# Kernel optimization log

Measured on AMD Instinct MI355X. Metric: run time of the kernel, lower is better.

The kernel has to match this reference:

```python
import jax, jax.numpy as jnp
import numpy as np

B, L, LQ = 64, 4096, 128
D = 32        # input_dim (value channels)
ET = 128      # embed_time
NH = 1        # num_heads
H = 128       # nhidden
NC = 6        # n_classes


def _time_emb(tt, lin_w, lin_b, per_w, per_b):
    # tt [..., T] -> [..., T, ET]; cat(Linear(1,1)(t), sin(Linear(1,ET-1)(t)))
    tt = tt[..., None]
    out1 = tt * lin_w[0, 0] + lin_b
    out2 = jnp.sin(tt @ per_w + per_b)
    return jnp.concatenate([out1, out2], axis=-1)


def _gru_dir(xs, wih, whh, bih, bhh, reverse):
    # xs [B, T, I] -> [B, T, H]; torch GRU gate math
    xs_t = jnp.swapaxes(xs, 0, 1)              # [T, B, I]
    if reverse:
        xs_t = xs_t[::-1]
    gi_all = xs_t @ wih.T + bih                # [T, B, 3H] precomputed input gates
    h0 = jnp.zeros((xs.shape[0], H), xs.dtype)

    def step(h, gi):
        gh = h @ whh.T + bhh
        ir, iz, inn = jnp.split(gi, 3, axis=-1)
        hr, hz, hn = jnp.split(gh, 3, axis=-1)
        r = jax.nn.sigmoid(ir + hr)
        z = jax.nn.sigmoid(iz + hz)
        n = jnp.tanh(inn + r * hn)
        h_new = (1.0 - z) * n + z * h
        return h_new, h_new

    _, ys = jax.lax.scan(step, h0, gi_all)     # [T, B, H]
    if reverse:
        ys = ys[::-1]
    return jnp.swapaxes(ys, 0, 1)


def _bigru(xs, wih, whh, bih, bhh):
    fwd = _gru_dir(xs, wih[0], whh[0], bih[0], bhh[0], False)
    bwd = _gru_dir(xs, wih[1], whh[1], bih[1], bhh[1], True)
    return jnp.concatenate([fwd, bwd], axis=-1)


def setup_inputs() -> dict:
    ks = jax.random.split(jax.random.key(0), 32)
    w = lambda i, s: jax.random.normal(ks[i], s, jnp.float32) * 0.05
    G3 = 3 * H
    return {
        "x": jax.random.normal(ks[0], (B, L, D), jnp.float32),
        "time_steps": jax.random.uniform(ks[1], (B, L), dtype=jnp.float32),
        "query_times": jnp.linspace(0.0, 1.0, LQ, dtype=jnp.float32),
        "lin_w": w(2, (1, 1)), "lin_b": w(3, (1,)),
        "per_w": w(4, (1, ET - 1)), "per_b": w(5, (ET - 1,)),
        "wq": w(6, (ET, ET)), "bq": w(7, (ET,)),
        "wk": w(8, (ET, ET)), "bk": w(9, (ET,)),
        "wo": w(10, (NH * D, H)), "bo": w(11, (H,)),
        "gru0_wih": w(12, (2, G3, H)), "gru0_whh": w(13, (2, G3, H)),
        "gru0_bih": w(14, (2, G3)), "gru0_bhh": w(15, (2, G3)),
        "gru1_wih": w(16, (2, G3, 2 * H)), "gru1_whh": w(17, (2, G3, H)),
        "gru1_bih": w(18, (2, G3)), "gru1_bhh": w(19, (2, G3)),
        "c1_w": w(20, (2 * H, 128)), "c1_b": w(21, (128,)),
        "c2_w": w(22, (128, 64)), "c2_b": w(23, (64,)),
        "c3_w": w(24, (64, NC)), "c3_b": w(25, (NC,)),
    }


def reference(x, time_steps, query_times, lin_w, lin_b, per_w, per_b,
              wq, bq, wk, bk, wo, bo,
              gru0_wih, gru0_whh, gru0_bih, gru0_bhh,
              gru1_wih, gru1_whh, gru1_bih, gru1_bhh,
              c1_w, c1_b, c2_w, c2_b, c3_w, c3_b):
    ek = ET // NH
    # learned time embeddings
    q = _time_emb(query_times[None, :], lin_w, lin_b, per_w, per_b)  # [1, LQ, ET]
    k = _time_emb(time_steps, lin_w, lin_b, per_w, per_b)            # [B, L, ET]
    # per-head projections
    qp = (q @ wq + bq).reshape(1, LQ, NH, ek).transpose(0, 2, 1, 3)[0]  # [NH, LQ, ek]
    kp = (k @ wk + bk).reshape(B, L, NH, ek).transpose(0, 2, 1, 3)      # [B, NH, L, ek]
    # mTAN attention: scores are channel-independent (mask=None), so the
    # per-channel repeat+softmax reduces to a single softmax over keys.
    scores = jnp.einsum('hqe,bhke->bhqk', qp, kp) / jnp.sqrt(jnp.float32(ek))
    p = jax.nn.softmax(scores, axis=-1)                                 # [B, NH, LQ, L]
    att = jnp.einsum('bhqk,bkd->bqhd', p, x).reshape(B, LQ, NH * D)
    att_out = att @ wo + bo                                             # [B, LQ, H]
    # 2-layer bidirectional GRU
    g0 = _bigru(att_out, gru0_wih, gru0_whh, gru0_bih, gru0_bhh)        # [B, LQ, 2H]
    g1 = _bigru(g0, gru1_wih, gru1_whh, gru1_bih, gru1_bhh)             # [B, LQ, 2H]
    class_in = jnp.concatenate([g1[:, -1, :H], g1[:, 0, H:]], axis=1)   # [B, 2H]
    out = ((class_in @ c1_w + c1_b) @ c2_w + c2_b) @ c3_w + c3_b        # [B, NC]
    return out
```

## Files before the change

kernel.cpp:

```cpp
#include <hip/hip_runtime.h>
#include <math.h>

#define Bn   64
#define Ln   4096
#define LQn  128
#define Dn   32
#define ETn  128
#define Hn   128
#define G3n  384
#define NDEG 12

typedef __attribute__((ext_vector_type(2))) float f32x2;
typedef __attribute__((ext_vector_type(2))) _Float16 f16x2;

#define DPPF(x, ctrl) __int_as_float(__builtin_amdgcn_update_dpp(0, __float_as_int(x), (ctrl), 0xF, 0xF, true))
#define QP_XOR1 0xB1
#define QP_XOR2 0x4E
#define QP_B0   0x00
#define QP_B1   0x55
#define QP_B2   0xAA
#define QP_B3   0xFF

__device__ __forceinline__ float sin_poly(float x) {
    const float x2 = x * x;
    float r = -1.9841270114e-04f;
    r = fmaf(r, x2,  8.3333337680e-03f);
    r = fmaf(r, x2, -1.6666667163e-01f);
    return fmaf(r * x2, x, x);
}
__device__ __forceinline__ float cos_poly(float x) {
    const float x2 = x * x;
    float r =  2.4801587642e-05f;
    r = fmaf(r, x2, -1.3888888899e-03f);
    r = fmaf(r, x2,  4.1666667908e-02f);
    r = fmaf(r, x2, -5.0000000000e-01f);
    return fmaf(r, x2, 1.0f);
}

#define WS_C    0
#define WS_WT   4096
#define WS_B2   (WS_WT + 768*32)
#define WS_CLS  (WS_B2 + 1024)
#define WS_G0   (WS_CLS + Bn*2*Hn)
#define WS_GI   (WS_G0 + Bn*LQn*2*Hn)
#define WS_ACCP WS_G0
#define WS_SP   (WS_G0 + 1048576)

__global__ __launch_bounds__(128) void k_coef(
    const float* __restrict__ qtimes, const float* __restrict__ lin_w,
    const float* __restrict__ lin_b, const float* __restrict__ per_w,
    const float* __restrict__ per_b, const float* __restrict__ wq,
    const float* __restrict__ bq, const float* __restrict__ wk,
    const float* __restrict__ bk, float* __restrict__ C)
{
    __shared__ float qe[ETn], qp_l[ETn], qt_l[ETn], bas[NDEG * 128], red[96], qbk_red[32];
    const int q = blockIdx.x, tid = threadIdx.x;
    if (tid < ETn - 1) {
        const float w = per_w[tid], bb = per_b[tid];
        const float sb = sin_poly(bb), cb = cos_poly(bb);
        float wp = 1.f;
#pragma unroll
        for (int d = 0; d < NDEG; ++d) {
            const float sd = ((d & 3) == 0) ? sb : ((d & 3) == 1) ? cb : ((d & 3) == 2) ? -sb : -cb;
            bas[d * 128 + tid] = wp * sd;
            wp *= w / (float)(d + 1);
        }
    }
    const float t = qtimes[q];
    qe[tid] = (tid == 0) ? fmaf(t, lin_w[0], lin_b[0])
                         : sin_poly(fmaf(t, per_w[tid - 1], per_b[tid - 1]));
    __syncthreads();
    {
        float a = bq[tid];
#pragma unroll 16
        for (int i = 0; i < ETn; ++i) a = fmaf(qe[i], wq[i * ETn + tid], a);
        qp_l[tid] = a;
    }
    __syncthreads();
    {
        const float4* wk4 = (const float4*)(wk + (size_t)tid * ETn);
        const float4* qp4 = (const float4*)qp_l;
        float a = 0.f;
#pragma unroll
        for (int k = 0; k < 32; ++k) {
            const float4 w4 = wk4[k], p4 = qp4[k];
            a += w4.x * p4.x + w4.y * p4.y + w4.z * p4.z + w4.w * p4.w;
        }
        qt_l[tid] = a;
    }
    __syncthreads();
    if (tid < 96) {
        const int d = tid >> 3, g = tid & 7;
        float p = 0.f;
        for (int j = g; j < ETn - 1; j += 8) p = fmaf(qt_l[j + 1], bas[d * 128 + j], p);
        red[tid] = p;
    } else {
        const int g2 = tid - 96;
        float p = 0.f;
#pragma unroll
        for (int k = 0; k < 4; ++k) p = fmaf(qp_l[g2 + 32 * k], bk[g2 + 32 * k], p);
        qbk_red[g2] = p;
    }
    __syncthreads();
    if (tid < NDEG) {
        const int d = tid;
        float s = red[d * 8 + 0] + red[d * 8 + 1] + red[d * 8 + 2] + red[d * 8 + 3]
                + red[d * 8 + 4] + red[d * 8 + 5] + red[d * 8 + 6] + red[d * 8 + 7];
        if (d == 0) {
            float qbk = 0.f;
#pragma unroll
            for (int k = 0; k < 32; ++k) qbk += qbk_red[k];
            s += qt_l[0] * lin_b[0] + qbk;
        }
        if (d == 1) s += qt_l[0] * lin_w[0];
        C[q * NDEG + d] = s * 0.08838834764831845f;
    }
}

__global__ __launch_bounds__(256) void k_fuse(
    const float* __restrict__ wih, const float* __restrict__ wo,
    const float* __restrict__ bo, const float* __restrict__ bih,
    float* __restrict__ Wt, float* __restrict__ bias2)
{
    const int t = blockIdx.x * 256 + threadIdx.x;
    if (t < 768 * 32) {
        const int o = t >> 5, d = t & 31;
        const float4* wr4 = (const float4*)(wih + (size_t)o * 128);
        const float4* wc4 = (const float4*)(wo + (size_t)d * 128);
        float a = 0.f;
#pragma unroll
        for (int k = 0; k < 32; ++k) {
            const float4 r4 = wr4[k], c4 = wc4[k];
            a += r4.x * c4.x + r4.y * c4.y + r4.z * c4.z + r4.w * c4.w;
        }
        Wt[t] = a;
    } else if (t < 768 * 33) {
        const int o = t - 768 * 32;
        const float4* wr4 = (const float4*)(wih + (size_t)o * 128);
        const float4* bo4 = (const float4*)bo;
        float a = bih[o];
#pragma unroll
        for (int k = 0; k < 32; ++k) {
            const float4 r4 = wr4[k], b4 = bo4[k];
            a += r4.x * b4.x + r4.y * b4.y + r4.z * b4.z + r4.w * b4.w;
        }
        bias2[o] = a;
    }
}

__global__ __launch_bounds__(512, 1) void k_attn(
    const float* __restrict__ x, const float* __restrict__ tsteps,
    const float* __restrict__ Cc, float* __restrict__ accP, float* __restrict__ sP)
{
    __shared__ float4 xls[4 * 64 * 8];
    __shared__ float  slab[4][128][36];
    const int tid = threadIdx.x;
    const int b = blockIdx.x >> 2, lsplit = blockIdx.x & 3;
    const int i = tid & 3, qt = (tid >> 2) & 31, ls2 = tid >> 7;
    const int qown = 4 * qt + i;
    const int u = tid & 127;

    float c[NDEG];
#pragma unroll
    for (int d = 0; d < NDEG; ++d) c[d] = Cc[qown * NDEG + d];

    const int l0 = lsplit * 1024 + ls2 * 256;
    const float4* tg4 = (const float4*)(tsteps + (size_t)b * Ln + l0);
    const float4* xg  = (const float4*)(x + ((size_t)b * Ln + l0) * Dn);

    f32x2 acc2[4][4];
#pragma unroll
    for (int m = 0; m < 4; ++m)
#pragma unroll
        for (int e = 0; e < 4; ++e) { acc2[m][e].x = 0.f; acc2[m][e].y = 0.f; }
    float s_own = 0.f;

    float4 xr[4];
#pragma unroll
    for (int w = 0; w < 4; ++w) xr[w] = xg[u + 128 * w];

    for (int ch = 0; ch < 4; ++ch) {
        __syncthreads();
#pragma unroll
        for (int w = 0; w < 4; ++w) xls[ls2 * 512 + u + 128 * w] = xr[w];
        __syncthreads();
        if (ch < 3) {
            const int off = (ch + 1) * 512;
#pragma unroll
            for (int w = 0; w < 4; ++w) xr[w] = xg[off + u + 128 * w];
        }
        const float4* xrow = &xls[ls2 * 512];
        for (int k = 0; k < 16; ++k) {
            const float4 t4 = tg4[ch * 16 + k];
#pragma unroll
            for (int jj = 0; jj < 4; ++jj) {
                const float t = (jj == 0) ? t4.x : (jj == 1) ? t4.y : (jj == 2) ? t4.z : t4.w;
                float sc = c[NDEG - 1];
#pragma unroll
                for (int d = NDEG - 2; d >= 0; --d) sc = fmaf(sc, t, c[d]);
                const float pe = __expf(sc);
                s_own += pe;
                const float p0 = DPPF(pe, QP_B0);
                const float p1 = DPPF(pe, QP_B1);
                const float p2 = DPPF(pe, QP_B2);
                const float p3 = DPPF(pe, QP_B3);
                const int lrow = (k * 4 + jj) * 8;
                const float4 xa = xrow[lrow + 2 * i];
                const float4 xb = xrow[lrow + 2 * i + 1];
                f32x2 xa0; xa0.x = xa.x; xa0.y = xa.y;
                f32x2 xa1; xa1.x = xa.z; xa1.y = xa.w;
                f32x2 xb0; xb0.x = xb.x; xb0.y = xb.y;
                f32x2 xb1; xb1.x = xb.z; xb1.y = xb.w;
#define PKA(m, pv) { f32x2 pp; pp.x = (pv); pp.y = (pv); \
    acc2[m][0] = __builtin_elementwise_fma(pp, xa0, acc2[m][0]); \
    acc2[m][1] = __builtin_elementwise_fma(pp, xa1, acc2[m][1]); \
    acc2[m][2] = __builtin_elementwise_fma(pp, xb0, acc2[m][2]); \
    acc2[m][3] = __builtin_elementwise_fma(pp, xb1, acc2[m][3]); }
                PKA(0, p0) PKA(1, p1) PKA(2, p2) PKA(3, p3)
#undef PKA
            }
        }
    }
    __syncthreads();
#pragma unroll
    for (int m = 0; m < 4; ++m) {
        float4 f4a, f4b;
        f4a.x = acc2[m][0].x; f4a.y = acc2[m][0].y; f4a.z = acc2[m][1].x; f4a.w = acc2[m][1].y;
        f4b.x = acc2[m][2].x; f4b.y = acc2[m][2].y; f4b.z = acc2[m][3].x; f4b.w = acc2[m][3].y;
        *(float4*)&slab[ls2][4 * qt + m][8 * i]     = f4a;
        *(float4*)&slab[ls2][4 * qt + m][8 * i + 4] = f4b;
    }
    slab[ls2][qown][32] = s_own;
    __syncthreads();
    const int q = tid & 127, part = tid >> 7;
#pragma unroll
    for (int j = 0; j < 2; ++j) {
        const int off = (part * 2 + j) * 4;
        float4 r  = *(float4*)&slab[0][q][off];
        float4 r1 = *(float4*)&slab[1][q][off];
        float4 r2 = *(float4*)&slab[2][q][off];
        float4 r3 = *(float4*)&slab[3][q][off];
        r.x += r1.x + r2.x + r3.x; r.y += r1.y + r2.y + r3.y;
        r.z += r1.z + r2.z + r3.z; r.w += r1.w + r2.w + r3.w;
        *(float4*)&accP[((((size_t)lsplit * Bn + b) * LQn + q) * 32) + off] = r;
    }
    if (part == 0) {
        sP[((size_t)lsplit * Bn + b) * LQn + q] =
            slab[0][q][32] + slab[1][q][32] + slab[2][q][32] + slab[3][q][32];
    }
}

__global__ __launch_bounds__(256) void k_gemm_att(
    const float* __restrict__ accP, const float* __restrict__ sP,
    const float* __restrict__ Bm, const float* __restrict__ bias,
    float* __restrict__ Cm)
{
    __shared__ float4 A_l[64 * 8];
    __shared__ float4 B_l[64 * 8];
    const int tid = threadIdx.x;
    const int m0 = blockIdx.x * 64, n0 = blockIdx.y * 64;
    const int r0 = (tid >> 4) << 2, c0 = (tid & 15) << 2;
    f32x2 acc2[4][4];
#pragma unroll
    for (int a = 0; a < 4; ++a)
#pragma unroll
        for (int bb = 0; bb < 4; ++bb) { acc2[a][bb].x = 0.f; acc2[a][bb].y = 0.f; }
    const float4* Ag = (const float4*)accP;
    const float4* Bg = (const float4*)Bm;

#pragma unroll
    for (int w = 0; w < 2; ++w) {
        const int idx = tid + w * 256;
        const int row = idx >> 3, c4 = idx & 7;
        const int sc = (c4 + row + (row >> 2)) & 7;
        const int m = m0 + row;
        float4 a0 = Ag[(size_t)m * 8 + c4];
        float4 a1 = Ag[((size_t)8192  + m) * 8 + c4];
        float4 a2 = Ag[((size_t)16384 + m) * 8 + c4];
        float4 a3 = Ag[((size_t)24576 + m) * 8 + c4];
        const float inv = 1.f / (sP[m] + sP[8192 + m] + sP[16384 + m] + sP[24576 + m]);
        float4 av;
        av.x = (a0.x + a1.x + a2.x + a3.x) * inv;
        av.y = (a0.y + a1.y + a2.y + a3.y) * inv;
        av.z = (a0.z + a1.z + a2.z + a3.z) * inv;
        av.w = (a0.w + a1.w + a2.w + a3.w) * inv;
        A_l[row * 8 + sc] = av;
        B_l[row * 8 + sc] = Bg[(size_t)(n0 + row) * 8 + c4];
    }
    __syncthreads();
#pragma unroll
    for (int k4 = 0; k4 < 8; ++k4) {
        float4 av[4], bv[4];
#pragma unroll
        for (int j = 0; j < 4; ++j) {
            const int ra = r0 + j;
            av[j] = A_l[ra * 8 + ((k4 + ra + (ra >> 2)) & 7)];
        }
#pragma unroll
        for (int j = 0; j < 4; ++j) {
            const int rb = c0 + j;
            bv[j] = B_l[rb * 8 + ((k4 + rb + (rb >> 2)) & 7)];
        }
#pragma unroll
        for (int ri = 0; ri < 4; ++ri) {
            f32x2 alo; alo.x = av[ri].x; alo.y = av[ri].y;
            f32x2 ahi; ahi.x = av[ri].z; ahi.y = av[ri].w;
#pragma unroll
            for (int ci = 0; ci < 4; ++ci) {
                f32x2 blo; blo.x = bv[ci].x; blo.y = bv[ci].y;
                f32x2 bhi; bhi.x = bv[ci].z; bhi.y = bv[ci].w;
                acc2[ri][ci] = __builtin_elementwise_fma(alo, blo, acc2[ri][ci]);
                acc2[ri][ci] = __builtin_elementwise_fma(ahi, bhi, acc2[ri][ci]);
            }
        }
    }
#pragma unroll
    for (int ri = 0; ri < 4; ++ri) {
        float4 o4;
        o4.x = acc2[ri][0].x + acc2[ri][0].y + bias[n0 + c0 + 0];
        o4.y = acc2[ri][1].x + acc2[ri][1].y + bias[n0 + c0 + 1];
        o4.z = acc2[ri][2].x + acc2[ri][2].y + bias[n0 + c0 + 2];
        o4.w = acc2[ri][3].x + acc2[ri][3].y + bias[n0 + c0 + 3];
        *(float4*)&Cm[(size_t)(m0 + r0 + ri) * 768 + n0 + c0] = o4;
    }
}

__global__ __launch_bounds__(256) void k_gemm_nt(
    const float* __restrict__ A, const float* __restrict__ Bm,
    const float* __restrict__ bias, float* __restrict__ Cm,
    int N, int K)
{
    __shared__ float4 A_l[64 * 8];
    __shared__ float4 B_l[64 * 8];
    const int tid = threadIdx.x;
    const int m0 = blockIdx.x * 64, n0 = blockIdx.y * 64;
    const int r0 = (tid >> 4) << 2, c0 = (tid & 15) << 2;
    const int K4 = K >> 2;
    f32x2 acc2[4][4];
#pragma unroll
    for (int a = 0; a < 4; ++a)
#pragma unroll
        for (int bb = 0; bb < 4; ++bb) { acc2[a][bb].x = 0.f; acc2[a][bb].y = 0.f; }
    const float4* Ag = (const float4*)A;
    const float4* Bg = (const float4*)Bm;

    for (int k0 = 0; k0 < K4; k0 += 8) {
        __syncthreads();
#pragma unroll
        for (int w = 0; w < 2; ++w) {
            const int idx = tid + w * 256;
            const int row = idx >> 3, c4 = idx & 7;
            const int sc = (c4 + row + (row >> 2)) & 7;
            A_l[row * 8 + sc] = Ag[(size_t)(m0 + row) * K4 + k0 + c4];
            B_l[row * 8 + sc] = Bg[(size_t)(n0 + row) * K4 + k0 + c4];
        }
        __syncthreads();
#pragma unroll
        for (int k4 = 0; k4 < 8; ++k4) {
            float4 av[4], bv[4];
#pragma unroll
            for (int j = 0; j < 4; ++j) {
                const int ra = r0 + j;
                av[j] = A_l[ra * 8 + ((k4 + ra + (ra >> 2)) & 7)];
            }
#pragma unroll
            for (int j = 0; j < 4; ++j) {
                const int rb = c0 + j;
                bv[j] = B_l[rb * 8 + ((k4 + rb + (rb >> 2)) & 7)];
            }
#pragma unroll
            for (int ri = 0; ri < 4; ++ri) {
                f32x2 alo; alo.x = av[ri].x; alo.y = av[ri].y;
                f32x2 ahi; ahi.x = av[ri].z; ahi.y = av[ri].w;
#pragma unroll
                for (int ci = 0; ci < 4; ++ci) {
                    f32x2 blo; blo.x = bv[ci].x; blo.y = bv[ci].y;
                    f32x2 bhi; bhi.x = bv[ci].z; bhi.y = bv[ci].w;
                    acc2[ri][ci] = __builtin_elementwise_fma(alo, blo, acc2[ri][ci]);
                    acc2[ri][ci] = __builtin_elementwise_fma(ahi, bhi, acc2[ri][ci]);
                }
            }
        }
    }
#pragma unroll
    for (int ri = 0; ri < 4; ++ri) {
        float4 o4;
        o4.x = acc2[ri][0].x + acc2[ri][0].y + bias[n0 + c0 + 0];
        o4.y = acc2[ri][1].x + acc2[ri][1].y + bias[n0 + c0 + 1];
        o4.z = acc2[ri][2].x + acc2[ri][2].y + bias[n0 + c0 + 2];
        o4.w = acc2[ri][3].x + acc2[ri][3].y + bias[n0 + c0 + 3];
        *(float4*)&Cm[(size_t)(m0 + r0 + ri) * N + n0 + c0] = o4;
    }
}

__global__ __launch_bounds__(256, 1) void k_gru(
    const float* __restrict__ gi, const float* __restrict__ whh,
    const float* __restrict__ bhh, float* __restrict__ seq_out,
    float* __restrict__ final_out)
{
    __shared__ _Float16 h16[2][Hn];
    __shared__ float    h32[2][Hn];
    const int tid = threadIdx.x;
    const int b = blockIdx.x >> 1, dir = blockIdx.x & 1;
    const int j = tid >> 1, q = tid & 1;

    f16x2 wr[32], wz[32], wn[32];
    {
        const float* wb = whh + ((size_t)dir * G3n + j) * Hn + 64 * q;
        const f32x2* p0 = (const f32x2*)(wb);
        const f32x2* p1 = (const f32x2*)(wb + (size_t)128 * Hn);
        const f32x2* p2 = (const f32x2*)(wb + (size_t)256 * Hn);
#pragma unroll
        for (int k = 0; k < 32; ++k) {
            f32x2 a = p0[k], z2 = p1[k], c2 = p2[k];
            wr[k].x = (_Float16)a.x;  wr[k].y = (_Float16)a.y;
            wz[k].x = (_Float16)z2.x; wz[k].y = (_Float16)z2.y;
            wn[k].x = (_Float16)c2.x; wn[k].y = (_Float16)c2.y;
        }
    }
#pragma unroll
    for (int k = 0; k < 32; ++k) {
        asm volatile("" : "+v"(wr[k]));
        asm volatile("" : "+v"(wz[k]));
        asm volatile("" : "+v"(wn[k]));
    }
    const float bhr = bhh[dir * G3n + j];
    const float bhz = bhh[dir * G3n + 128 + j];
    const float bhn = bhh[dir * G3n + 256 + j];

    if (tid < Hn) {
        h32[0][tid] = 0.f; h32[1][tid] = 0.f;
        h16[0][tid] = (_Float16)0.f; h16[1][tid] = (_Float16)0.f;
    }
    __syncthreads();

    const long sstride = dir ? -768 : 768;
    const float* gptr = gi + (size_t)b * LQn * 768 + dir * G3n + j
                        + (size_t)(dir ? LQn - 1 : 0) * 768;

    int cur = 0;
    float hlast = 0.f;

    auto gstep = [&](const float gir, const float giz, const float gin, const int step) {
        const float hold = h32[cur][j];
        const float4* hb4 = (const float4*)(&h16[cur][64 * q]);
        float sr = 0.f, sz = 0.f, sn = 0.f;
#pragma unroll
        for (int k2 = 0; k2 < 8; ++k2) {
            float4 hv = hb4[k2];
            f16x2 h0 = *(f16x2*)&hv.x;
            f16x2 h1 = *(f16x2*)&hv.y;
            f16x2 h2 = *(f16x2*)&hv.z;
            f16x2 h3 = *(f16x2*)&hv.w;
            asm("v_dot2_f32_f16 %0, %1, %2, %0" : "+v"(sr) : "v"(wr[4 * k2 + 0]), "v"(h0));
            asm("v_dot2_f32_f16 %0, %1, %2, %0" : "+v"(sz) : "v"(wz[4 * k2 + 0]), "v"(h0));
            asm("v_dot2_f32_f16 %0, %1, %2, %0" : "+v"(sn) : "v"(wn[4 * k2 + 0]), "v"(h0));
            asm("v_dot2_f32_f16 %0, %1, %2, %0" : "+v"(sr) : "v"(wr[4 * k2 + 1]), "v"(h1));
            asm("v_dot2_f32_f16 %0, %1, %2, %0" : "+v"(sz) : "v"(wz[4 * k2 + 1]), "v"(h1));
            asm("v_dot2_f32_f16 %0, %1, %2, %0" : "+v"(sn) : "v"(wn[4 * k2 + 1]), "v"(h1));
            asm("v_dot2_f32_f16 %0, %1, %2, %0" : "+v"(sr) : "v"(wr[4 * k2 + 2]), "v"(h2));
            asm("v_dot2_f32_f16 %0, %1, %2, %0" : "+v"(sz) : "v"(wz[4 * k2 + 2]), "v"(h2));
            asm("v_dot2_f32_f16 %0, %1, %2, %0" : "+v"(sn) : "v"(wn[4 * k2 + 2]), "v"(h2));
            asm("v_dot2_f32_f16 %0, %1, %2, %0" : "+v"(sr) : "v"(wr[4 * k2 + 3]), "v"(h3));
            asm("v_dot2_f32_f16 %0, %1, %2, %0" : "+v"(sz) : "v"(wz[4 * k2 + 3]), "v"(h3));
            asm("v_dot2_f32_f16 %0, %1, %2, %0" : "+v"(sn) : "v"(wn[4 * k2 + 3]), "v"(h3));
        }
        sr += DPPF(sr, QP_XOR1);
        sz += DPPF(sz, QP_XOR1);
        sn += DPPF(sn, QP_XOR1);
        const float r = 1.f / (1.f + __expf(-(gir + sr + bhr)));
        const float z = 1.f / (1.f + __expf(-(giz + sz + bhz)));
        const float nx = gin + r * (sn + bhn);
        const float n = 1.f - 2.f / (1.f + __expf(2.f * nx));
        const float hn = n + z * (hold - n);
        if (q == 0) {
            h32[cur ^ 1][j] = hn;
            h16[cur ^ 1][j] = (_Float16)hn;
            if (seq_out) {
                const int l = dir ? (LQn - 1 - step) : step;
                seq_out[((size_t)(b * LQn + l)) * (2 * Hn) + dir * Hn + j] = hn;
            }
        }
        hlast = hn;
        cur ^= 1;
        asm volatile("s_waitcnt lgkmcnt(0)\n\ts_barrier" ::: "memory");
    };

    float gA[3], gB[3];
#define GLD(dst, s) { const long o = (long)(s) * sstride; \
    dst[0] = gptr[o]; dst[1] = gptr[o + 128]; dst[2] = gptr[o + 256]; }
    GLD(gA, 0) GLD(gB, 1)
    for (int s0 = 0; s0 < LQn; s0 += 2) {
        gstep(gA[0], gA[1], gA[2], s0);
        { const int sn2 = (s0 + 2 < LQn) ? s0 + 2 : LQn - 1; GLD(gA, sn2) }
        gstep(gB[0], gB[1], gB[2], s0 + 1);
        { const int sn2 = (s0 + 3 < LQn) ? s0 + 3 : LQn - 1; GLD(gB, sn2) }
    }
#undef GLD
    if (final_out && q == 0) final_out[b * 2 * Hn + dir * Hn + j] = hlast;
}

__global__ __launch_bounds__(256) void k_cls(
    const float* __restrict__ cls_in,
    const float* __restrict__ c1w, const float* __restrict__ c1b,
    const float* __restrict__ c2w, const float* __restrict__ c2b,
    const float* __restrict__ c3w, const float* __restrict__ c3b,
    float* __restrict__ out)
{
    __shared__ float ci[256], y1[128], y2[64];
    const int b = blockIdx.x, tid = threadIdx.x;
    ci[tid] = cls_in[b * 256 + tid];
    __syncthreads();
    if (tid < 128) { float a = c1b[tid]; for (int i = 0; i < 256; ++i) a += ci[i] * c1w[i * 128 + tid]; y1[tid] = a; }
    __syncthreads();
    if (tid < 64)  { float a = c2b[tid]; for (int i = 0; i < 128; ++i) a += y1[i] * c2w[i * 64 + tid];  y2[tid] = a; }
    __syncthreads();
    if (tid < 6)   { float a = c3b[tid]; for (int i = 0; i < 64; ++i)  a += y2[i] * c3w[i * 6 + tid];   out[b * 6 + tid] = a; }
}

extern "C" void kernel_launch(void* const* d_in, const int* in_sizes, int n_in,
                              void* d_out, int out_size, void* d_ws, size_t ws_size,
                              hipStream_t stream)
{
    const float* x        = (const float*)d_in[0];
    const float* tsteps   = (const float*)d_in[1];
    const float* qtimes   = (const float*)d_in[2];
    const float* lin_w    = (const float*)d_in[3];
    const float* lin_b    = (const float*)d_in[4];
    const float* per_w    = (const float*)d_in[5];
    const float* per_b    = (const float*)d_in[6];
    const float* wq       = (const float*)d_in[7];
    const float* bq       = (const float*)d_in[8];
    const float* wk       = (const float*)d_in[9];
    const float* bk       = (const float*)d_in[10];
    const float* wo       = (const float*)d_in[11];
    const float* bo       = (const float*)d_in[12];
    const float* g0_wih   = (const float*)d_in[13];
    const float* g0_whh   = (const float*)d_in[14];
    const float* g0_bih   = (const float*)d_in[15];
    const float* g0_bhh   = (const float*)d_in[16];
    const float* g1_wih   = (const float*)d_in[17];
    const float* g1_whh   = (const float*)d_in[18];
    const float* g1_bih   = (const float*)d_in[19];
    const float* g1_bhh   = (const float*)d_in[20];
    const float* c1w      = (const float*)d_in[21];
    const float* c1b      = (const float*)d_in[22];
    const float* c2w      = (const float*)d_in[23];
    const float* c2b      = (const float*)d_in[24];
    const float* c3w      = (const float*)d_in[25];
    const float* c3b      = (const float*)d_in[26];
    float* out = (float*)d_out;
    float* ws  = (float*)d_ws;

    float* Cws   = ws + WS_C;
    float* Wt    = ws + WS_WT;
    float* bias2 = ws + WS_B2;
    float* clsin = ws + WS_CLS;
    float* g0buf = ws + WS_G0;
    float* accP  = ws + WS_ACCP;
    float* sPb   = ws + WS_SP;
    float* gibuf = ws + WS_GI;

    k_coef<<<128, 128, 0, stream>>>(qtimes, lin_w, lin_b, per_w, per_b, wq, bq, wk, bk, Cws);
    k_fuse<<<99, 256, 0, stream>>>(g0_wih, wo, bo, g0_bih, Wt, bias2);
    k_attn<<<256, 512, 0, stream>>>(x, tsteps, Cws, accP, sPb);

    k_gemm_att<<<dim3(128, 12), 256, 0, stream>>>(accP, sPb, Wt, bias2, gibuf);
    k_gru<<<128, 256, 0, stream>>>(gibuf, g0_whh, g0_bhh, g0buf, nullptr);

    k_gemm_nt<<<dim3(128, 12), 256, 0, stream>>>(g0buf, g1_wih, g1_bih, gibuf, 768, 256);
    k_gru<<<128, 256, 0, stream>>>(gibuf, g1_whh, g1_bhh, nullptr, clsin);

    k_cls<<<64, 256, 0, stream>>>(clsin, c1w, c1b, c2w, c2b, c3w, c3b, out);
}
```

Baseline: 302.3 us.

## Process two batch rows per GRU block and union attention shared memory

The GRU kernel now handles two batch elements per block. Each pair of lanes computes dot products for both batch rows against the same register-resident weights, and each lane then finalises the gates for its own row, so the grid halves from 128 to 64 blocks and the weight-load cost is shared. The attention kernel aliases its x staging buffer and its reduction slab into one shared-memory region and raises the launch-bounds occupancy hint to 4, lowering LDS use per block. The trade-off is twice the dot-product work per step in the latency-bound GRU recurrence, and the aliasing is correct only if the staging buffer is no longer read once the slab is written.

```diff
diff --git a/kernel.cpp b/kernel.cpp
--- a/kernel.cpp
+++ b/kernel.cpp
@@ -148,12 +148,14 @@
     }
 }
 
-__global__ __launch_bounds__(512, 1) void k_attn(
+__global__ __launch_bounds__(512, 4) void k_attn(
     const float* __restrict__ x, const float* __restrict__ tsteps,
     const float* __restrict__ Cc, float* __restrict__ accP, float* __restrict__ sP)
 {
-    __shared__ float4 xls[4 * 64 * 8];
-    __shared__ float  slab[4][128][36];
+    __shared__ __align__(16) char smem[4 * 128 * 36 * 4];
+    float4* xls  = (float4*)smem;
+    float*  slabf = (float*)smem;
+#define SLAB(s, qq, c) slabf[(((s) * 128) + (qq)) * 36 + (c)]
     const int tid = threadIdx.x;
     const int b = blockIdx.x >> 2, lsplit = blockIdx.x & 3;
     const int i = tid & 3, qt = (tid >> 2) & 31, ls2 = tid >> 7;
@@ -227,27 +229,28 @@
         float4 f4a, f4b;
         f4a.x = acc2[m][0].x; f4a.y = acc2[m][0].y; f4a.z = acc2[m][1].x; f4a.w = acc2[m][1].y;
         f4b.x = acc2[m][2].x; f4b.y = acc2[m][2].y; f4b.z = acc2[m][3].x; f4b.w = acc2[m][3].y;
-        *(float4*)&slab[ls2][4 * qt + m][8 * i]     = f4a;
-        *(float4*)&slab[ls2][4 * qt + m][8 * i + 4] = f4b;
-    }
-    slab[ls2][qown][32] = s_own;
+        *(float4*)&SLAB(ls2, 4 * qt + m, 8 * i)     = f4a;
+        *(float4*)&SLAB(ls2, 4 * qt + m, 8 * i + 4) = f4b;
+    }
+    SLAB(ls2, qown, 32) = s_own;
     __syncthreads();
     const int q = tid & 127, part = tid >> 7;
 #pragma unroll
     for (int j = 0; j < 2; ++j) {
         const int off = (part * 2 + j) * 4;
-        float4 r  = *(float4*)&slab[0][q][off];
-        float4 r1 = *(float4*)&slab[1][q][off];
-        float4 r2 = *(float4*)&slab[2][q][off];
-        float4 r3 = *(float4*)&slab[3][q][off];
+        float4 r  = *(float4*)&SLAB(0, q, off);
+        float4 r1 = *(float4*)&SLAB(1, q, off);
+        float4 r2 = *(float4*)&SLAB(2, q, off);
+        float4 r3 = *(float4*)&SLAB(3, q, off);
         r.x += r1.x + r2.x + r3.x; r.y += r1.y + r2.y + r3.y;
         r.z += r1.z + r2.z + r3.z; r.w += r1.w + r2.w + r3.w;
         *(float4*)&accP[((((size_t)lsplit * Bn + b) * LQn + q) * 32) + off] = r;
     }
     if (part == 0) {
         sP[((size_t)lsplit * Bn + b) * LQn + q] =
-            slab[0][q][32] + slab[1][q][32] + slab[2][q][32] + slab[3][q][32];
-    }
+            SLAB(0, q, 32) + SLAB(1, q, 32) + SLAB(2, q, 32) + SLAB(3, q, 32);
+    }
+#undef SLAB
 }
 
 __global__ __launch_bounds__(256) void k_gemm_att(
@@ -398,11 +401,12 @@
     const float* __restrict__ bhh, float* __restrict__ seq_out,
     float* __restrict__ final_out)
 {
-    __shared__ _Float16 h16[2][Hn];
-    __shared__ float    h32[2][Hn];
+    __shared__ _Float16 h16[2][2][Hn];
+    __shared__ float    h32[2][2][Hn];
     const int tid = threadIdx.x;
-    const int b = blockIdx.x >> 1, dir = blockIdx.x & 1;
+    const int bg = blockIdx.x >> 1, dir = blockIdx.x & 1;
     const int j = tid >> 1, q = tid & 1;
+    const int b = bg * 2 + q;
 
     f16x2 wr[32], wz[32], wn[32];
     {
@@ -428,58 +432,69 @@
     const float bhz = bhh[dir * G3n + 128 + j];
     const float bhn = bhh[dir * G3n + 256 + j];
 
-    if (tid < Hn) {
-        h32[0][tid] = 0.f; h32[1][tid] = 0.f;
-        h16[0][tid] = (_Float16)0.f; h16[1][tid] = (_Float16)0.f;
-    }
+    ((float*)h32)[tid] = 0.f;      ((float*)h32)[tid + 256] = 0.f;
+    ((_Float16*)h16)[tid] = (_Float16)0.f; ((_Float16*)h16)[tid + 256] = (_Float16)0.f;
     __syncthreads();
 
     const long sstride = dir ? -768 : 768;
-    const float* gptr = gi + (size_t)b * LQn * 768 + dir * G3n + j
-                        + (size_t)(dir ? LQn - 1 : 0) * 768;
+    const float* gptr = gi + ((size_t)b * LQn + (size_t)(dir ? LQn - 1 : 0)) * 768
+                        + dir * G3n + j;
 
     int cur = 0;
     float hlast = 0.f;
 
-    auto gstep = [&](const float gir, const float giz, const float gin, const int step) {
-        const float hold = h32[cur][j];
-        const float4* hb4 = (const float4*)(&h16[cur][64 * q]);
-        float sr = 0.f, sz = 0.f, sn = 0.f;
+    auto gstep = [&](const float g0, const float g1, const float g2, const int step) {
+        const float hold = h32[cur][q][j];
+        const float4* hb0 = (const float4*)(&h16[cur][0][64 * q]);
+        const float4* hb1 = (const float4*)(&h16[cur][1][64 * q]);
+        float sr0 = 0.f, sz0 = 0.f, sn0 = 0.f;
+        float sr1 = 0.f, sz1 = 0.f, sn1 = 0.f;
 #pragma unroll
         for (int k2 = 0; k2 < 8; ++k2) {
-            float4 hv = hb4[k2];
-            f16x2 h0 = *(f16x2*)&hv.x;
-            f16x2 h1 = *(f16x2*)&hv.y;
-            f16x2 h2 = *(f16x2*)&hv.z;
-            f16x2 h3 = *(f16x2*)&hv.w;
-            asm("v_dot2_f32_f16 %0, %1, %2, %0" : "+v"(sr) : "v"(wr[4 * k2 + 0]), "v"(h0));
-            asm("v_dot2_f32_f16 %0, %1, %2, %0" : "+v"(sz) : "v"(wz[4 * k2 + 0]), "v"(h0));
-            asm("v_dot2_f32_f16 %0, %1, %2, %0" : "+v"(sn) : "v"(wn[4 * k2 + 0]), "v"(h0));
-            asm("v_dot2_f32_f16 %0, %1, %2, %0" : "+v"(sr) : "v"(wr[4 * k2 + 1]), "v"(h1));
-            asm("v_dot2_f32_f16 %0, %1, %2, %0" : "+v"(sz) : "v"(wz[4 * k2 + 1]), "v"(h1));
-            asm("v_dot2_f32_f16 %0, %1, %2, %0" : "+v"(sn) : "v"(wn[4 * k2 + 1]), "v"(h1));
-            asm("v_dot2_f32_f16 %0, %1, %2, %0" : "+v"(sr) : "v"(wr[4 * k2 + 2]), "v"(h2));
-            asm("v_dot2_f32_f16 %0, %1, %2, %0" : "+v"(sz) : "v"(wz[4 * k2 + 2]), "v"(h2));
-            asm("v_dot2_f32_f16 %0, %1, %2, %0" : "+v"(sn) : "v"(wn[4 * k2 + 2]), "v"(h2));
-            asm("v_dot2_f32_f16 %0, %1, %2, %0" : "+v"(sr) : "v"(wr[4 * k2 + 3]), "v"(h3));
-            asm("v_dot2_f32_f16 %0, %1, %2, %0" : "+v"(sz) : "v"(wz[4 * k2 + 3]), "v"(h3));
-            asm("v_dot2_f32_f16 %0, %1, %2, %0" : "+v"(sn) : "v"(wn[4 * k2 + 3]), "v"(h3));
-        }
-        sr += DPPF(sr, QP_XOR1);
-        sz += DPPF(sz, QP_XOR1);
-        sn += DPPF(sn, QP_XOR1);
-        const float r = 1.f / (1.f + __expf(-(gir + sr + bhr)));
-        const float z = 1.f / (1.f + __expf(-(giz + sz + bhz)));
-        const float nx = gin + r * (sn + bhn);
+            const float4 v0 = hb0[k2];
+            const float4 v1 = hb1[k2];
+            f16x2 a0 = *(f16x2*)&v0.x, a1 = *(f16x2*)&v0.y, a2 = *(f16x2*)&v0.z, a3 = *(f16x2*)&v0.w;
+            f16x2 c0 = *(f16x2*)&v1.x, c1 = *(f16x2*)&v1.y, c2 = *(f16x2*)&v1.z, c3 = *(f16x2*)&v1.w;
+            asm("v_dot2_f32_f16 %0, %1, %2, %0" : "+v"(sr0) : "v"(wr[4 * k2 + 0]), "v"(a0));
+            asm("v_dot2_f32_f16 %0, %1, %2, %0" : "+v"(sz0) : "v"(wz[4 * k2 + 0]), "v"(a0));
+            asm("v_dot2_f32_f16 %0, %1, %2, %0" : "+v"(sn0) : "v"(wn[4 * k2 + 0]), "v"(a0));
+            asm("v_dot2_f32_f16 %0, %1, %2, %0" : "+v"(sr1) : "v"(wr[4 * k2 + 0]), "v"(c0));
+            asm("v_dot2_f32_f16 %0, %1, %2, %0" : "+v"(sz1) : "v"(wz[4 * k2 + 0]), "v"(c0));
+            asm("v_dot2_f32_f16 %0, %1, %2, %0" : "+v"(sn1) : "v"(wn[4 * k2 + 0]), "v"(c0));
+            asm("v_dot2_f32_f16 %0, %1, %2, %0" : "+v"(sr0) : "v"(wr[4 * k2 + 1]), "v"(a1));
+            asm("v_dot2_f32_f16 %0, %1, %2, %0" : "+v"(sz0) : "v"(wz[4 * k2 + 1]), "v"(a1));
+            asm("v_dot2_f32_f16 %0, %1, %2, %0" : "+v"(sn0) : "v"(wn[4 * k2 + 1]), "v"(a1));
+            asm("v_dot2_f32_f16 %0, %1, %2, %0" : "+v"(sr1) : "v"(wr[4 * k2 + 1]), "v"(c1));
+            asm("v_dot2_f32_f16 %0, %1, %2, %0" : "+v"(sz1) : "v"(wz[4 * k2 + 1]), "v"(c1));
+            asm("v_dot2_f32_f16 %0, %1, %2, %0" : "+v"(sn1) : "v"(wn[4 * k2 + 1]), "v"(c1));
+            asm("v_dot2_f32_f16 %0, %1, %2, %0" : "+v"(sr0) : "v"(wr[4 * k2 + 2]), "v"(a2));
+            asm("v_dot2_f32_f16 %0, %1, %2, %0" : "+v"(sz0) : "v"(wz[4 * k2 + 2]), "v"(a2));
+            asm("v_dot2_f32_f16 %0, %1, %2, %0" : "+v"(sn0) : "v"(wn[4 * k2 + 2]), "v"(a2));
+            asm("v_dot2_f32_f16 %0, %1, %2, %0" : "+v"(sr1) : "v"(wr[4 * k2 + 2]), "v"(c2));
+            asm("v_dot2_f32_f16 %0, %1, %2, %0" : "+v"(sz1) : "v"(wz[4 * k2 + 2]), "v"(c2));
+            asm("v_dot2_f32_f16 %0, %1, %2, %0" : "+v"(sn1) : "v"(wn[4 * k2 + 2]), "v"(c2));
+            asm("v_dot2_f32_f16 %0, %1, %2, %0" : "+v"(sr0) : "v"(wr[4 * k2 + 3]), "v"(a3));
+            asm("v_dot2_f32_f16 %0, %1, %2, %0" : "+v"(sz0) : "v"(wz[4 * k2 + 3]), "v"(a3));
+            asm("v_dot2_f32_f16 %0, %1, %2, %0" : "+v"(sn0) : "v"(wn[4 * k2 + 3]), "v"(a3));
+            asm("v_dot2_f32_f16 %0, %1, %2, %0" : "+v"(sr1) : "v"(wr[4 * k2 + 3]), "v"(c3));
+            asm("v_dot2_f32_f16 %0, %1, %2, %0" : "+v"(sz1) : "v"(wz[4 * k2 + 3]), "v"(c3));
+            asm("v_dot2_f32_f16 %0, %1, %2, %0" : "+v"(sn1) : "v"(wn[4 * k2 + 3]), "v"(c3));
+        }
+        sr0 += DPPF(sr0, QP_XOR1); sz0 += DPPF(sz0, QP_XOR1); sn0 += DPPF(sn0, QP_XOR1);
+        sr1 += DPPF(sr1, QP_XOR1); sz1 += DPPF(sz1, QP_XOR1); sn1 += DPPF(sn1, QP_XOR1);
+        const float sr = q ? sr1 : sr0;
+        const float sz = q ? sz1 : sz0;
+        const float sn = q ? sn1 : sn0;
+        const float r = 1.f / (1.f + __expf(-(g0 + sr + bhr)));
+        const float z = 1.f / (1.f + __expf(-(g1 + sz + bhz)));
+        const float nx = g2 + r * (sn + bhn);
         const float n = 1.f - 2.f / (1.f + __expf(2.f * nx));
         const float hn = n + z * (hold - n);
-        if (q == 0) {
-            h32[cur ^ 1][j] = hn;
-            h16[cur ^ 1][j] = (_Float16)hn;
-            if (seq_out) {
-                const int l = dir ? (LQn - 1 - step) : step;
-                seq_out[((size_t)(b * LQn + l)) * (2 * Hn) + dir * Hn + j] = hn;
-            }
+        h32[cur ^ 1][q][j] = hn;
+        h16[cur ^ 1][q][j] = (_Float16)hn;
+        if (seq_out) {
+            const int l = dir ? (LQn - 1 - step) : step;
+            seq_out[((size_t)(b * LQn + l)) * (2 * Hn) + dir * Hn + j] = hn;
         }
         hlast = hn;
         cur ^= 1;
@@ -497,7 +512,7 @@
         { const int sn2 = (s0 + 3 < LQn) ? s0 + 3 : LQn - 1; GLD(gB, sn2) }
     }
 #undef GLD
-    if (final_out && q == 0) final_out[b * 2 * Hn + dir * Hn + j] = hlast;
+    if (final_out) final_out[b * 2 * Hn + dir * Hn + j] = hlast;
 }
 
 __global__ __launch_bounds__(256) void k_cls(
@@ -566,10 +581,10 @@
     k_attn<<<256, 512, 0, stream>>>(x, tsteps, Cws, accP, sPb);
 
     k_gemm_att<<<dim3(128, 12), 256, 0, stream>>>(accP, sPb, Wt, bias2, gibuf);
-    k_gru<<<128, 256, 0, stream>>>(gibuf, g0_whh, g0_bhh, g0buf, nullptr);
+    k_gru<<<64, 256, 0, stream>>>(gibuf, g0_whh, g0_bhh, g0buf, nullptr);
 
     k_gemm_nt<<<dim3(128, 12), 256, 0, stream>>>(g0buf, g1_wih, g1_bih, gibuf, 768, 256);
-    k_gru<<<128, 256, 0, stream>>>(gibuf, g1_whh, g1_bhh, nullptr, clsin);
+    k_gru<<<64, 256, 0, stream>>>(gibuf, g1_whh, g1_bhh, nullptr, clsin);
 
     k_cls<<<64, 256, 0, stream>>>(clsin, c1w, c1b, c2w, c2b, c3w, c3b, out);
 }
```

Measured after the change: 452.6 us. 49.7% more time.
